# Performance work log

Measured on AMD Instinct MI355X. Metric: run time of the kernel, lower is better.

The kernel has to match this reference:

```python
import jax, jax.numpy as jnp
import numpy as np

B = 256          # batch == num_blocks
SEQ = 128
HIDDEN = 1024
NUM_BLOCKS = 256
NUM_LABELS = 3


def setup_inputs() -> dict:
    key = jax.random.key(0)
    k1, k2, k3, k4 = jax.random.split(key, 4)
    entity_encoding = jax.random.normal(k1, (B, SEQ, HIDDEN), dtype=jnp.float32)
    states = jax.random.normal(k2, (B, NUM_BLOCKS * HIDDEN), dtype=jnp.float32)
    H_w = jax.random.normal(k3, (HIDDEN, HIDDEN), dtype=jnp.float32) * (1.0 / np.sqrt(HIDDEN))
    R_w = jax.random.normal(k4, (NUM_LABELS, HIDDEN), dtype=jnp.float32) * (1.0 / np.sqrt(HIDDEN))
    prelu_alpha = jnp.ones((HIDDEN,), dtype=jnp.float32)  # init=1.0
    return {"entity_encoding": entity_encoding, "states": states,
            "H_w": H_w, "R_w": R_w, "prelu_alpha": prelu_alpha}


def reference(entity_encoding, states, H_w, R_w, prelu_alpha):
    # x: CLS token, [B, H]
    x = entity_encoding[:, 0, :]
    # states -> [B, num_blocks, H]; chunk i of torch.chunk(..., dim=1) is S[:, i, :]
    S = states.reshape(B, NUM_BLOCKS, HIDDEN)
    # per-block dot with x, softmax over the batch axis (dim=0 in torch)
    scores = jnp.einsum('bh,bkh->bk', x, S)          # [B, nb]
    p = jax.nn.softmax(scores, axis=0)               # softmax over b
    # u[k] = sum_b p[b,k] * S[b,k,:]  -> [nb, H]; nb == B
    u = jnp.einsum('bk,bkh->kh', p, S)
    v = x + u @ H_w.T                                # [B, H]
    act = jnp.where(v >= 0, v, prelu_alpha * v)      # PReLU, per-channel alpha
    return act @ R_w.T                               # [B, num_labels]
```

## Files before the change

### kernel.cpp

```cpp
#include <hip/hip_runtime.h>
#include <math.h>

#define B_DIM 256
#define K_DIM 256
#define H_DIM 1024
#define SEQ_DIM 128
#define L_DIM 3
#define NSPLIT 8
#define BS (B_DIM / NSPLIT)
#define SK 4

__global__ __launch_bounds__(64) void k_flash(const float* __restrict__ ent,
                                              const float* __restrict__ S,
                                              float* __restrict__ num,
                                              float* __restrict__ ml) {
    int k = blockIdx.x, sp = blockIdx.y, lane = threadIdx.x;
    int b0 = sp * BS;

    const float* Sp = S   + ((size_t)(b0 * K_DIM + k)) * H_DIM;
    const float* Xp = ent + (size_t)b0 * SEQ_DIM * H_DIM;

    float4 acc[4] = {{0,0,0,0},{0,0,0,0},{0,0,0,0},{0,0,0,0}};
    float m = -INFINITY, l = 0.f;

    float4 sc[4], xc[4];
#pragma unroll
    for (int r = 0; r < 4; ++r) {
        int idx = r * 256 + lane * 4;
        sc[r] = *(const float4*)(Sp + idx);
        xc[r] = *(const float4*)(Xp + idx);
    }

    for (int bb = 0; bb < BS; ++bb) {
        float4 sn[4] = {{0,0,0,0},{0,0,0,0},{0,0,0,0},{0,0,0,0}};
        float4 xn[4] = {{0,0,0,0},{0,0,0,0},{0,0,0,0},{0,0,0,0}};
        if (bb + 1 < BS) {
            const float* Snp = Sp + (size_t)(bb + 1) * K_DIM * H_DIM;
            const float* Xnp = Xp + (size_t)(bb + 1) * SEQ_DIM * H_DIM;
#pragma unroll
            for (int r = 0; r < 4; ++r) {
                int idx = r * 256 + lane * 4;
                sn[r] = *(const float4*)(Snp + idx);
                xn[r] = *(const float4*)(Xnp + idx);
            }
        }
        float partial = 0.f;
#pragma unroll
        for (int r = 0; r < 4; ++r)
            partial += sc[r].x * xc[r].x + sc[r].y * xc[r].y
                     + sc[r].z * xc[r].z + sc[r].w * xc[r].w;
#pragma unroll
        for (int off = 1; off < 64; off <<= 1)
            partial += __shfl_xor(partial, off, 64);
        float s = partial;

        float mn = fmaxf(m, s);
        float scale = expf(m - mn);
        float e = expf(s - mn);
#pragma unroll
        for (int r = 0; r < 4; ++r) {
            acc[r].x = acc[r].x * scale + e * sc[r].x;
            acc[r].y = acc[r].y * scale + e * sc[r].y;
            acc[r].z = acc[r].z * scale + e * sc[r].z;
            acc[r].w = acc[r].w * scale + e * sc[r].w;
        }
        l = l * scale + e;
        m = mn;
#pragma unroll
        for (int r = 0; r < 4; ++r) { sc[r] = sn[r]; xc[r] = xn[r]; }
    }

    float* np = num + ((size_t)(sp * K_DIM + k)) * H_DIM;
#pragma unroll
    for (int r = 0; r < 4; ++r)
        *(float4*)(np + r * 256 + lane * 4) = acc[r];
    if (lane == 0) {
        ml[sp * K_DIM + k] = m;
        ml[NSPLIT * K_DIM + sp * K_DIM + k] = l;
    }
}

__global__ void k_combine(const float* __restrict__ num, const float* __restrict__ ml,
                          float* __restrict__ u) {
    int k = blockIdx.x, t = threadIdx.x;
    float M = -INFINITY;
#pragma unroll
    for (int sp = 0; sp < NSPLIT; ++sp) M = fmaxf(M, ml[sp * K_DIM + k]);
    float w[NSPLIT];
    float denom = 0.f;
#pragma unroll
    for (int sp = 0; sp < NSPLIT; ++sp) {
        w[sp] = expf(ml[sp * K_DIM + k] - M);
        denom += w[sp] * ml[NSPLIT * K_DIM + sp * K_DIM + k];
    }
    float inv = 1.f / denom;
    float4 a = {0.f, 0.f, 0.f, 0.f};
#pragma unroll
    for (int sp = 0; sp < NSPLIT; ++sp) {
        float4 n4 = *(const float4*)(num + ((size_t)(sp * K_DIM + k)) * H_DIM + t * 4);
        a.x += w[sp] * n4.x; a.y += w[sp] * n4.y; a.z += w[sp] * n4.z; a.w += w[sp] * n4.w;
    }
    a.x *= inv; a.y *= inv; a.z *= inv; a.w *= inv;
    *(float4*)(u + (size_t)k * H_DIM + t * 4) = a;
}

__global__ void k_vgemm(const float* __restrict__ u, const float* __restrict__ Hw,
                        float* __restrict__ vpart) {
    __shared__ float Us[64][17];
    __shared__ float Hs[64][17];
    int tid = threadIdx.x;
    int tx = tid & 15, ty = tid >> 4;
    int hx = blockIdx.x * 64, by = blockIdx.y * 64, z = blockIdx.z;
    float acc[4][4] = {};
    int li = tid * 4;
    int r = li >> 4, cc = li & 15;
    int k0 = z * (H_DIM / SK), k1 = k0 + (H_DIM / SK);
    for (int kk0 = k0; kk0 < k1; kk0 += 16) {
        float4 uv = *(const float4*)(u  + (size_t)(by + r) * H_DIM + kk0 + cc);
        float4 hv = *(const float4*)(Hw + (size_t)(hx + r) * H_DIM + kk0 + cc);
        Us[r][cc] = uv.x; Us[r][cc + 1] = uv.y; Us[r][cc + 2] = uv.z; Us[r][cc + 3] = uv.w;
        Hs[r][cc] = hv.x; Hs[r][cc + 1] = hv.y; Hs[r][cc + 2] = hv.z; Hs[r][cc + 3] = hv.w;
        __syncthreads();
#pragma unroll
        for (int kk = 0; kk < 16; ++kk) {
            float a[4], bv[4];
#pragma unroll
            for (int i = 0; i < 4; ++i) a[i]  = Us[ty * 4 + i][kk];
#pragma unroll
            for (int j = 0; j < 4; ++j) bv[j] = Hs[tx * 4 + j][kk];
#pragma unroll
            for (int i = 0; i < 4; ++i)
#pragma unroll
                for (int j = 0; j < 4; ++j) acc[i][j] += a[i] * bv[j];
        }
        __syncthreads();
    }
#pragma unroll
    for (int i = 0; i < 4; ++i) {
        int b = by + ty * 4 + i;
#pragma unroll
        for (int j = 0; j < 4; ++j) {
            int h = hx + tx * 4 + j;
            vpart[((size_t)z * B_DIM + b) * H_DIM + h] = acc[i][j];
        }
    }
}

__global__ void k_final(const float* __restrict__ vpart, const float* __restrict__ ent,
                        const float* __restrict__ alpha, const float* __restrict__ Rw,
                        float* __restrict__ out) {
    __shared__ float sm[4 * L_DIM];
    int b = blockIdx.x, t = threadIdx.x;
    int lane = t & 63, wave = t >> 6;
    float4 v = *(const float4*)(ent + (size_t)b * SEQ_DIM * H_DIM + t * 4);
#pragma unroll
    for (int z = 0; z < SK; ++z) {
        float4 p4 = *(const float4*)(vpart + ((size_t)z * B_DIM + b) * H_DIM + t * 4);
        v.x += p4.x; v.y += p4.y; v.z += p4.z; v.w += p4.w;
    }
    float4 al = *(const float4*)(alpha + t * 4);
    v.x = (v.x >= 0.f) ? v.x : al.x * v.x;
    v.y = (v.y >= 0.f) ? v.y : al.y * v.y;
    v.z = (v.z >= 0.f) ? v.z : al.z * v.z;
    v.w = (v.w >= 0.f) ? v.w : al.w * v.w;
    float p[L_DIM];
#pragma unroll
    for (int l = 0; l < L_DIM; ++l) {
        float4 r4 = *(const float4*)(Rw + l * H_DIM + t * 4);
        p[l] = v.x * r4.x + v.y * r4.y + v.z * r4.z + v.w * r4.w;
    }
#pragma unroll
    for (int off = 32; off > 0; off >>= 1) {
#pragma unroll
        for (int l = 0; l < L_DIM; ++l) p[l] += __shfl_down(p[l], off, 64);
    }
    if (lane == 0) {
#pragma unroll
        for (int l = 0; l < L_DIM; ++l) sm[wave * L_DIM + l] = p[l];
    }
    __syncthreads();
    if (t < L_DIM) {
        out[b * L_DIM + t] = sm[t] + sm[L_DIM + t] + sm[2 * L_DIM + t] + sm[3 * L_DIM + t];
    }
}

extern "C" void kernel_launch(void* const* d_in, const int* in_sizes, int n_in,
                              void* d_out, int out_size, void* d_ws, size_t ws_size,
                              hipStream_t stream) {
    const float* ent   = (const float*)d_in[0];
    const float* S     = (const float*)d_in[1];
    const float* Hw    = (const float*)d_in[2];
    const float* Rw    = (const float*)d_in[3];
    const float* alpha = (const float*)d_in[4];
    float* out = (float*)d_out;

    float* ws    = (float*)d_ws;
    float* num   = ws;
    float* ml    = num + (size_t)NSPLIT * K_DIM * H_DIM;
    float* u     = ml + 2 * NSPLIT * K_DIM;
    float* vpart = u + (size_t)K_DIM * H_DIM;

    k_flash  <<<dim3(K_DIM, NSPLIT), 64, 0, stream>>>(ent, S, num, ml);
    k_combine<<<K_DIM, 256, 0, stream>>>(num, ml, u);
    k_vgemm  <<<dim3(H_DIM / 64, B_DIM / 64, SK), 256, 0, stream>>>(u, Hw, vpart);
    k_final  <<<B_DIM, 256, 0, stream>>>(vpart, ent, alpha, Rw, out);
}
```

Measured before the change: 439.4 us.

## Raise split counts, use nontemporal S loads, vectorize vgemm shared-memory tiles

Doubles the batch split of the streaming softmax kernel to 16 and the K split of the GEMM to 8, creating more blocks for the bandwidth-bound pass over S. Switches S and partial-numerator loads to nontemporal loads and adds launch-bound occupancy hints. Transposes the vgemm shared-memory tiles so each thread reads float4 vectors and writes float4 outputs. In exchange it doubles the partial-numerator and vpart workspace and adds more combine and reduction work.

```diff
diff --git a/kernel.cpp b/kernel.cpp
--- a/kernel.cpp
+++ b/kernel.cpp
@@ -6,14 +6,21 @@
 #define H_DIM 1024
 #define SEQ_DIM 128
 #define L_DIM 3
-#define NSPLIT 8
+#define NSPLIT 16
 #define BS (B_DIM / NSPLIT)
-#define SK 4
-
-__global__ __launch_bounds__(64) void k_flash(const float* __restrict__ ent,
-                                              const float* __restrict__ S,
-                                              float* __restrict__ num,
-                                              float* __restrict__ ml) {
+#define SK 8
+
+typedef float vfloat4 __attribute__((ext_vector_type(4)));
+
+__device__ __forceinline__ float4 ntload4(const float* p) {
+    vfloat4 v = __builtin_nontemporal_load((const vfloat4*)p);
+    return make_float4(v.x, v.y, v.z, v.w);
+}
+
+__global__ __launch_bounds__(64, 4) void k_flash(const float* __restrict__ ent,
+                                                 const float* __restrict__ S,
+                                                 float* __restrict__ num,
+                                                 float* __restrict__ ml) {
     int k = blockIdx.x, sp = blockIdx.y, lane = threadIdx.x;
     int b0 = sp * BS;
 
@@ -27,7 +34,7 @@
 #pragma unroll
     for (int r = 0; r < 4; ++r) {
         int idx = r * 256 + lane * 4;
-        sc[r] = *(const float4*)(Sp + idx);
+        sc[r] = ntload4(Sp + idx);
         xc[r] = *(const float4*)(Xp + idx);
     }
 
@@ -40,7 +47,7 @@
 #pragma unroll
             for (int r = 0; r < 4; ++r) {
                 int idx = r * 256 + lane * 4;
-                sn[r] = *(const float4*)(Snp + idx);
+                sn[r] = ntload4(Snp + idx);
                 xn[r] = *(const float4*)(Xnp + idx);
             }
         }
@@ -97,52 +104,47 @@
     float4 a = {0.f, 0.f, 0.f, 0.f};
 #pragma unroll
     for (int sp = 0; sp < NSPLIT; ++sp) {
-        float4 n4 = *(const float4*)(num + ((size_t)(sp * K_DIM + k)) * H_DIM + t * 4);
+        float4 n4 = ntload4(num + ((size_t)(sp * K_DIM + k)) * H_DIM + t * 4);
         a.x += w[sp] * n4.x; a.y += w[sp] * n4.y; a.z += w[sp] * n4.z; a.w += w[sp] * n4.w;
     }
     a.x *= inv; a.y *= inv; a.z *= inv; a.w *= inv;
     *(float4*)(u + (size_t)k * H_DIM + t * 4) = a;
 }
 
-__global__ void k_vgemm(const float* __restrict__ u, const float* __restrict__ Hw,
-                        float* __restrict__ vpart) {
-    __shared__ float Us[64][17];
-    __shared__ float Hs[64][17];
+__global__ __launch_bounds__(256, 2) void k_vgemm(const float* __restrict__ u,
+                                                  const float* __restrict__ Hw,
+                                                  float* __restrict__ vpart) {
+    __shared__ float Us[16][68];
+    __shared__ float Hs[16][68];
     int tid = threadIdx.x;
     int tx = tid & 15, ty = tid >> 4;
     int hx = blockIdx.x * 64, by = blockIdx.y * 64, z = blockIdx.z;
     float acc[4][4] = {};
-    int li = tid * 4;
-    int r = li >> 4, cc = li & 15;
-    int k0 = z * (H_DIM / SK), k1 = k0 + (H_DIM / SK);
-    for (int kk0 = k0; kk0 < k1; kk0 += 16) {
+    int r = tid >> 2, cc = (tid & 3) * 4;
+    int k0 = z * (H_DIM / SK);
+    for (int kt = 0; kt < H_DIM / SK; kt += 16) {
+        int kk0 = k0 + kt;
         float4 uv = *(const float4*)(u  + (size_t)(by + r) * H_DIM + kk0 + cc);
         float4 hv = *(const float4*)(Hw + (size_t)(hx + r) * H_DIM + kk0 + cc);
-        Us[r][cc] = uv.x; Us[r][cc + 1] = uv.y; Us[r][cc + 2] = uv.z; Us[r][cc + 3] = uv.w;
-        Hs[r][cc] = hv.x; Hs[r][cc + 1] = hv.y; Hs[r][cc + 2] = hv.z; Hs[r][cc + 3] = hv.w;
+        Us[cc + 0][r] = uv.x; Us[cc + 1][r] = uv.y; Us[cc + 2][r] = uv.z; Us[cc + 3][r] = uv.w;
+        Hs[cc + 0][r] = hv.x; Hs[cc + 1][r] = hv.y; Hs[cc + 2][r] = hv.z; Hs[cc + 3][r] = hv.w;
         __syncthreads();
 #pragma unroll
         for (int kk = 0; kk < 16; ++kk) {
-            float a[4], bv[4];
-#pragma unroll
-            for (int i = 0; i < 4; ++i) a[i]  = Us[ty * 4 + i][kk];
-#pragma unroll
-            for (int j = 0; j < 4; ++j) bv[j] = Hs[tx * 4 + j][kk];
-#pragma unroll
-            for (int i = 0; i < 4; ++i)
-#pragma unroll
-                for (int j = 0; j < 4; ++j) acc[i][j] += a[i] * bv[j];
+            float4 av = *(const float4*)&Us[kk][ty * 4];
+            float4 bv = *(const float4*)&Hs[kk][tx * 4];
+            acc[0][0] += av.x * bv.x; acc[0][1] += av.x * bv.y; acc[0][2] += av.x * bv.z; acc[0][3] += av.x * bv.w;
+            acc[1][0] += av.y * bv.x; acc[1][1] += av.y * bv.y; acc[1][2] += av.y * bv.z; acc[1][3] += av.y * bv.w;
+            acc[2][0] += av.z * bv.x; acc[2][1] += av.z * bv.y; acc[2][2] += av.z * bv.z; acc[2][3] += av.z * bv.w;
+            acc[3][0] += av.w * bv.x; acc[3][1] += av.w * bv.y; acc[3][2] += av.w * bv.z; acc[3][3] += av.w * bv.w;
         }
         __syncthreads();
     }
 #pragma unroll
     for (int i = 0; i < 4; ++i) {
         int b = by + ty * 4 + i;
-#pragma unroll
-        for (int j = 0; j < 4; ++j) {
-            int h = hx + tx * 4 + j;
-            vpart[((size_t)z * B_DIM + b) * H_DIM + h] = acc[i][j];
-        }
+        float4 o = {acc[i][0], acc[i][1], acc[i][2], acc[i][3]};
+        *(float4*)(vpart + ((size_t)z * B_DIM + b) * H_DIM + hx + tx * 4) = o;
     }
 }
 
```

Result: faster. 420.7 us (-4.3%).
